# Performance work log

Hardware: AMD Instinct MI355X
Metric: run time of the kernel (lower is better)

Reference implementation:

```python
import jax, jax.numpy as jnp
import numpy as np

N = 4096        # batch size (rows)
K = 4           # instances per class -> num_instances in the torch code
D = 256         # embedding dim
MARGIN = 0.5
SAMPLE_KEY = jax.random.key(42)  # fixed key: deterministic stand-in for torch.multinomial


def setup_inputs() -> dict:
    key = jax.random.key(0)
    x = jax.random.normal(key, (N, D), dtype=jnp.float32)
    # L2-normalize like typical metric-learning embeddings so sims are in [-1, 1]
    inputs = x / jnp.linalg.norm(x, axis=1, keepdims=True)
    targets = (jnp.arange(N) // K).astype(jnp.int32)  # P*K batch: equal-size classes
    return {"inputs": inputs, "targets": targets}


def reference(inputs, targets):
    n = inputs.shape[0]
    km1 = K - 1                 # positives per row
    n_neg = n - K               # negatives per row

    sim = inputs @ inputs.T                                   # [n, n]
    same = targets[:, None] == targets[None, :]
    eye = jnp.eye(n, dtype=bool)
    pos_mask = same & ~eye
    neg_mask = ~same

    # masked_select + per-row sort: masked entries -> +inf, ascending sort,
    # keep first count entries (counts are uniform across rows)
    pos_sorted = jnp.sort(jnp.where(pos_mask, sim, jnp.inf), axis=1)[:, :km1]   # [n, K-1]
    neg_sorted = jnp.sort(jnp.where(neg_mask, sim, jnp.inf), axis=1)[:, :n_neg] # [n, n-K]

    pos_d = jnp.mean(pos_sorted)
    neg_d = jnp.mean(neg_sorted)

    # GaussDistribution per row over negatives
    neg_mean = jnp.mean(neg_sorted, axis=1, keepdims=True)
    neg_std = jnp.sqrt(jnp.mean((neg_sorted - neg_mean) ** 2, axis=1, keepdims=True))
    # NOTE: the original uses exp(+(x-mu)^2 / (2 sigma^2)) (no minus sign) -- faithful
    logprob = (neg_sorted - neg_mean) ** 2 / (2.0 * neg_std ** 2)               # [n, n-K]

    # multinomial without replacement ~ Gumbel top-k on log-weights
    gumbel = -jnp.log(-jnp.log(
        jax.random.uniform(SAMPLE_KEY, logprob.shape, minval=1e-20, maxval=1.0)))
    _, neg_idx = jax.lax.top_k(logprob + gumbel, km1)                            # [n, K-1]
    neg_pair = jnp.take_along_axis(neg_sorted, neg_idx, axis=1)                  # [n, K-1]

    pos_loss = jnp.mean(jnp.log1p(jnp.exp(-2.0 * (pos_sorted - MARGIN))), axis=1)
    neg_loss = 0.04 * jnp.mean(jnp.log1p(jnp.exp(50.0 * (neg_pair - MARGIN))), axis=1)
    loss = jnp.sum(pos_loss + neg_loss) / n

    # prec: fraction of rows where hardest positive > hardest sampled negative + 0.05
    c = jnp.sum(pos_sorted[:, -1] > jnp.max(neg_pair, axis=1) + 0.05)
    prec = c.astype(jnp.float32) / n

    return loss, prec, pos_d, neg_d
```

## Files before the change

kernel.cpp:

```cpp
#include <hip/hip_runtime.h>
#include <hip/hip_bf16.h>
#include <cstdint>
#include <cfloat>
#include <math.h>

#define NN 4096
#define DD 256
#define NNEG 4092
#define MARGIN 0.5f
#define NB 3584
#define NW (NB / 2)

__device__ __forceinline__ uint32_t rotl32(uint32_t x, int r) {
  return (x << r) | (x >> (32 - r));
}

__device__ __forceinline__ void threefry2x32_42(uint32_t x0, uint32_t x1,
                                                uint32_t& o0, uint32_t& o1) {
  const uint32_t k0 = 0u, k1 = 42u;
  const uint32_t k2 = k0 ^ k1 ^ 0x1BD11BDAu;
  x0 += k0; x1 += k1;
#define TF_R(r) { x0 += x1; x1 = rotl32(x1, r); x1 ^= x0; }
  TF_R(13) TF_R(15) TF_R(26) TF_R(6)
  x0 += k1; x1 += k2 + 1u;
  TF_R(17) TF_R(29) TF_R(16) TF_R(24)
  x0 += k2; x1 += k0 + 2u;
  TF_R(13) TF_R(15) TF_R(26) TF_R(6)
  x0 += k0; x1 += k1 + 3u;
  TF_R(17) TF_R(29) TF_R(16) TF_R(24)
  x0 += k1; x1 += k2 + 4u;
  TF_R(13) TF_R(15) TF_R(26) TF_R(6)
  x0 += k2; x1 += k0 + 5u;
#undef TF_R
  o0 = x0; o1 = x1;
}

__device__ __forceinline__ float gumbel_at(uint32_t f) {
  uint32_t o0, o1;
  threefry2x32_42(0u, f, o0, o1);
  uint32_t bits = o0 ^ o1;
  uint32_t fb = (bits >> 9) | 0x3F800000u;
  float fl = __uint_as_float(fb) - 1.0f;
  float u = fmaxf(1e-20f, fl + 1e-20f);
  return -logf(-logf(u));
}

__device__ __forceinline__ int bucket_of(float v) {
  return (int)fminf(fmaxf((v + 0.5f) * (float)NB, 0.0f), (float)(NB - 1));
}

#define BT 128
#define NT (NN / BT)
#define BK 32
#define LDSS 36

__global__ __launch_bounds__(256) void gemm_sim(const float* __restrict__ X,
                                                float* __restrict__ S) {
  __shared__ float As[BT * LDSS];
  __shared__ float Bs[BT * LDSS];
  const int tid = threadIdx.x;
  const int tx = tid & 15, ty = tid >> 4;

  int b = blockIdx.x, bi = 0;
  while (b >= NT - bi) { b -= NT - bi; bi++; }
  const int bj = bi + b;
  const int rowBase = bi * BT, colBase = bj * BT;

  float acc[8][8] = {};
  for (int kb = 0; kb < DD; kb += BK) {
#pragma unroll
    for (int it = 0; it < 4; ++it) {
      int idx = tid + 256 * it;
      int r = idx >> 3, c4 = idx & 7;
      float4 av = *(const float4*)(X + (size_t)(rowBase + r) * DD + kb + c4 * 4);
      float4 bv = *(const float4*)(X + (size_t)(colBase + r) * DD + kb + c4 * 4);
      *(float4*)(As + r * LDSS + c4 * 4) = av;
      *(float4*)(Bs + r * LDSS + c4 * 4) = bv;
    }
    __syncthreads();
    for (int k = 0; k < BK; k += 4) {
      float4 a[8], bfr[8];
#pragma unroll
      for (int i = 0; i < 8; ++i) a[i] = *(const float4*)(As + (ty + 16 * i) * LDSS + k);
#pragma unroll
      for (int j = 0; j < 8; ++j) bfr[j] = *(const float4*)(Bs + (tx + 16 * j) * LDSS + k);
#pragma unroll
      for (int i = 0; i < 8; ++i)
#pragma unroll
        for (int j = 0; j < 8; ++j) {
          acc[i][j] += a[i].x * bfr[j].x;
          acc[i][j] += a[i].y * bfr[j].y;
          acc[i][j] += a[i].z * bfr[j].z;
          acc[i][j] += a[i].w * bfr[j].w;
        }
    }
    __syncthreads();
  }
#pragma unroll
  for (int i = 0; i < 8; ++i)
#pragma unroll
    for (int j = 0; j < 8; ++j)
      S[(size_t)(rowBase + ty + 16 * i) * NN + colBase + tx + 16 * j] = acc[i][j];
  if (bi != bj) {
#pragma unroll
    for (int i = 0; i < 8; ++i)
#pragma unroll
      for (int j = 0; j < 8; ++j)
        S[(size_t)(colBase + tx + 16 * j) * NN + rowBase + ty + 16 * i] = acc[i][j];
  }
}

#define INSERT3(sc, v)                                              \
  if ((sc) > s2) {                                                  \
    if ((sc) > s1) {                                                \
      s2 = s1; v2 = v1;                                             \
      if ((sc) > s0) { s1 = s0; v1 = v0; s0 = (sc); v0 = (v); }     \
      else           { s1 = (sc); v1 = (v); }                       \
    } else { s2 = (sc); v2 = (v); }                                 \
  }

__global__ __launch_bounds__(256) void row_kernel(const float* __restrict__ S,
                                                  float* __restrict__ acc) {
  __shared__ uint32_t histw[NW];
  __shared__ uint32_t offsw[NW];
  __shared__ float sval[NN];
  __shared__ float sh[48];
  __shared__ uint32_t wtot[4];

  const int row = blockIdx.x;
  const int tid = threadIdx.x;
  const int lane = tid & 63, wid = tid >> 6;

#pragma unroll
  for (int i = 0; i < 7; ++i) histw[tid + 256 * i] = 0u;

  const float4* src = (const float4*)(S + (size_t)row * NN);
  const int pslot = row >> 2;
  float vv[16];
#pragma unroll
  for (int it = 0; it < 4; ++it) {
    int slot = tid + 256 * it;
    float4 t4 = src[slot];
    if (slot == pslot) {
      sh[16] = t4.x; sh[17] = t4.y; sh[18] = t4.z; sh[19] = t4.w;
      t4.x = INFINITY; t4.y = INFINITY; t4.z = INFINITY; t4.w = INFINITY;
    }
    vv[4 * it + 0] = t4.x; vv[4 * it + 1] = t4.y;
    vv[4 * it + 2] = t4.z; vv[4 * it + 3] = t4.w;
  }

  float s = 0.0f;
#pragma unroll
  for (int e = 0; e < 16; ++e) if (vv[e] < 1e30f) s += vv[e];
#pragma unroll
  for (int off = 32; off > 0; off >>= 1) s += __shfl_down(s, off, 64);
  if (lane == 0) sh[5 + wid] = s;
  __syncthreads();

#pragma unroll
  for (int e = 0; e < 16; ++e) {
    int b = bucket_of(vv[e]);
    atomicAdd(&histw[b >> 1], 1u << ((b & 1) << 4));
  }
  if (tid == 0) {
    int self = row & 3;
    float p[3]; int m = 0;
#pragma unroll
    for (int c = 0; c < 4; ++c)
      if (c != self) p[m++] = sh[16 + c];
    float t;
    if (p[0] > p[1]) { t = p[0]; p[0] = p[1]; p[1] = t; }
    if (p[1] > p[2]) { t = p[1]; p[1] = p[2]; p[2] = t; }
    if (p[0] > p[1]) { t = p[0]; p[0] = p[1]; p[1] = t; }
    sh[0] = p[0]; sh[1] = p[1]; sh[2] = p[2];
    float tot = sh[5] + sh[6] + sh[7] + sh[8];
    sh[9] = tot;
    sh[3] = tot / (float)NNEG;
  }
  __syncthreads();

  uint32_t hw[7];
  uint32_t s14 = 0;
#pragma unroll
  for (int j = 0; j < 7; ++j) {
    hw[j] = histw[7 * tid + j];
    s14 += (hw[j] & 0xFFFFu) + (hw[j] >> 16);
  }
  uint32_t inc = s14;
#pragma unroll
  for (int off = 1; off < 64; off <<= 1) {
    uint32_t n = __shfl_up(inc, (unsigned)off, 64);
    if (lane >= off) inc += n;
  }
  if (lane == 63) wtot[wid] = inc;

  const float mu = sh[3];
  float q = 0.0f;
#pragma unroll
  for (int e = 0; e < 16; ++e)
    if (vv[e] < 1e30f) { float d = vv[e] - mu; q += d * d; }
#pragma unroll
  for (int off = 32; off > 0; off >>= 1) q += __shfl_down(q, off, 64);
  if (lane == 0) sh[10 + wid] = q;
  __syncthreads();

  uint32_t wbase = 0;
  for (int w = 0; w < wid; ++w) wbase += wtot[w];
  uint32_t run = wbase + inc - s14;
#pragma unroll
  for (int j = 0; j < 7; ++j) {
    uint32_t lo = run; run += hw[j] & 0xFFFFu;
    uint32_t hi = run; run += hw[j] >> 16;
    offsw[7 * tid + j] = lo | (hi << 16);
  }
  if (tid == 0) {
    float var = (sh[10] + sh[11] + sh[12] + sh[13]) / (float)NNEG;
    float sd = sqrtf(var);
    sh[4] = 1.0f / (2.0f * sd * sd);
  }
  __syncthreads();

#pragma unroll
  for (int e = 0; e < 16; ++e) {
    int b = bucket_of(vv[e]);
    uint32_t old = atomicAdd(&offsw[b >> 1], 1u << ((b & 1) << 4));
    uint32_t sl = (old >> ((b & 1) << 4)) & 0xFFFFu;
    sval[sl] = vv[e];
  }
  __syncthreads();

  const float inv2s2 = sh[4];
  const uint32_t fbase = (uint32_t)row * (uint32_t)NNEG;
  float s0 = -FLT_MAX, s1 = -FLT_MAX, s2 = -FLT_MAX;
  float v0 = 0.0f, v1 = 0.0f, v2 = 0.0f;
#pragma unroll 1
  for (int it = 0; it < 16; ++it) {
    int sl = tid + 256 * it;
    float v = sval[sl];
    if (v < 1e30f) {
      int b = bucket_of(v);
      uint32_t sh16 = (uint32_t)((b & 1) << 4);
      uint32_t end = (offsw[b >> 1] >> sh16) & 0xFFFFu;
      uint32_t cntb = (histw[b >> 1] >> sh16) & 0xFFFFu;
      uint32_t st = end - cntb;
      int cnt = (int)st;
      for (uint32_t u = st; u < end; ++u) {
        float w = sval[u];
        cnt += (w < v || (w == v && (int)u < sl)) ? 1 : 0;
      }
      float d = v - mu;
      float sc = d * d * inv2s2 + gumbel_at(fbase + (uint32_t)cnt);
      INSERT3(sc, v)
    }
  }

#pragma unroll
  for (int dlt = 1; dlt < 64; dlt <<= 1) {
    float t0 = __shfl_xor(s0, dlt, 64), u0 = __shfl_xor(v0, dlt, 64);
    float t1 = __shfl_xor(s1, dlt, 64), u1 = __shfl_xor(v1, dlt, 64);
    float t2 = __shfl_xor(s2, dlt, 64), u2 = __shfl_xor(v2, dlt, 64);
    INSERT3(t0, u0)
    INSERT3(t1, u1)
    INSERT3(t2, u2)
  }
  if (lane == 0) {
    int b0 = 24 + wid * 6;
    sh[b0 + 0] = s0; sh[b0 + 1] = v0;
    sh[b0 + 2] = s1; sh[b0 + 3] = v1;
    sh[b0 + 4] = s2; sh[b0 + 5] = v2;
  }
  __syncthreads();

  if (tid == 0) {
    float g0 = -FLT_MAX, g1 = -FLT_MAX, g2 = -FLT_MAX;
    float w0 = 0.0f, w1 = 0.0f, w2 = 0.0f;
    {
      float s0 = g0, s1 = g1, s2 = g2, v0 = w0, v1 = w1, v2 = w2;
#pragma unroll
      for (int i = 0; i < 12; ++i) {
        float sc = sh[24 + 2 * i], v = sh[24 + 2 * i + 1];
        INSERT3(sc, v)
      }
      g0 = s0; g1 = s1; g2 = s2; w0 = v0; w1 = v1; w2 = v2;
    }
    float negmax = fmaxf(w0, fmaxf(w1, w2));
    float neg_loss = 0.04f * (log1pf(expf(50.0f * (w0 - MARGIN))) +
                              log1pf(expf(50.0f * (w1 - MARGIN))) +
                              log1pf(expf(50.0f * (w2 - MARGIN)))) / 3.0f;
    float p0 = sh[0], p1 = sh[1], p2 = sh[2];
    float pos_loss = (log1pf(expf(-2.0f * (p0 - MARGIN))) +
                      log1pf(expf(-2.0f * (p1 - MARGIN))) +
                      log1pf(expf(-2.0f * (p2 - MARGIN)))) / 3.0f;
    atomicAdd(&acc[0], pos_loss + neg_loss);
    if (p2 > negmax + 0.05f) atomicAdd(&acc[1], 1.0f);
    atomicAdd(&acc[2], p0 + p1 + p2);
    atomicAdd(&acc[3], sh[9]);
  }
}

__global__ void finalize(const float* __restrict__ acc, float* out) {
  if (threadIdx.x == 0 && blockIdx.x == 0) {
    out[0] = acc[0] / 4096.0f;
    out[1] = acc[1] / 4096.0f;
    out[2] = acc[2] / (4096.0f * 3.0f);
    out[3] = acc[3] / (4096.0f * 4092.0f);
  }
}

extern "C" void kernel_launch(void* const* d_in, const int* in_sizes, int n_in,
                              void* d_out, int out_size, void* d_ws, size_t ws_size,
                              hipStream_t stream) {
  (void)in_sizes; (void)n_in; (void)out_size; (void)ws_size;
  const float* X = (const float*)d_in[0];
  float* S = (float*)d_ws;
  float* acc = (float*)((char*)d_ws + (size_t)NN * NN * 4);
  hipMemsetAsync(acc, 0, 4 * sizeof(float), stream);
  gemm_sim<<<NT * (NT + 1) / 2, 256, 0, stream>>>(X, S);
  row_kernel<<<NN, 256, 0, stream>>>(S, acc);
  finalize<<<1, 64, 0, stream>>>(acc, (float*)d_out);
}
```

Before: 372.1 us.

## Precompute Gumbel noise table alongside GEMM and gather it in row kernel

Adds extra blocks to the GEMM launch that fill a full N×(N-K) table of Gumbel noise while the similarity GEMM runs. The row kernel then gathers the noise by rank instead of running threefry plus two logs per element, and its loop is split into a rank-count phase and a scoring phase to batch the loads. This swaps per-row transcendental compute for about 67MB of extra global writes and reads. The path runs only if the workspace is large enough, otherwise it falls back to generating noise inline.

```diff
diff --git a/kernel.cpp b/kernel.cpp
--- a/kernel.cpp
+++ b/kernel.cpp
@@ -53,12 +53,24 @@
 #define NT (NN / BT)
 #define BK 32
 #define LDSS 36
-
-__global__ __launch_bounds__(256) void gemm_sim(const float* __restrict__ X,
-                                                float* __restrict__ S) {
+#define GEMM_BLOCKS (NT * (NT + 1) / 2)
+#define GUMBEL_BLOCKS 240
+#define GTOTAL ((uint32_t)NN * (uint32_t)NNEG)
+
+__global__ __launch_bounds__(256) void gemm_gumbel(const float* __restrict__ X,
+                                                   float* __restrict__ S,
+                                                   float* __restrict__ G) {
   __shared__ float As[BT * LDSS];
   __shared__ float Bs[BT * LDSS];
   const int tid = threadIdx.x;
+
+  if (blockIdx.x >= GEMM_BLOCKS) {
+    uint32_t i = (uint32_t)(blockIdx.x - GEMM_BLOCKS) * 256u + (uint32_t)tid;
+    const uint32_t stride = (uint32_t)GUMBEL_BLOCKS * 256u;
+    for (; i < GTOTAL; i += stride) G[i] = gumbel_at(i);
+    return;
+  }
+
   const int tx = tid & 15, ty = tid >> 4;
 
   int b = blockIdx.x, bi = 0;
@@ -119,7 +131,9 @@
     } else { s2 = (sc); v2 = (v); }                                 \
   }
 
+template <int USE_G>
 __global__ __launch_bounds__(256) void row_kernel(const float* __restrict__ S,
+                                                  const float* __restrict__ G,
                                                   float* __restrict__ acc) {
   __shared__ uint32_t histw[NW];
   __shared__ uint32_t offsw[NW];
@@ -231,25 +245,38 @@
 
   const float inv2s2 = sh[4];
   const uint32_t fbase = (uint32_t)row * (uint32_t)NNEG;
+  const float* __restrict__ Grow = G + fbase;
   float s0 = -FLT_MAX, s1 = -FLT_MAX, s2 = -FLT_MAX;
   float v0 = 0.0f, v1 = 0.0f, v2 = 0.0f;
-#pragma unroll 1
+  float vr[16]; uint32_t cr[16];
+#pragma unroll
   for (int it = 0; it < 16; ++it) {
     int sl = tid + 256 * it;
     float v = sval[sl];
+    uint32_t cnt = 0u;
     if (v < 1e30f) {
       int b = bucket_of(v);
       uint32_t sh16 = (uint32_t)((b & 1) << 4);
       uint32_t end = (offsw[b >> 1] >> sh16) & 0xFFFFu;
       uint32_t cntb = (histw[b >> 1] >> sh16) & 0xFFFFu;
       uint32_t st = end - cntb;
-      int cnt = (int)st;
+      int c = (int)st;
       for (uint32_t u = st; u < end; ++u) {
         float w = sval[u];
-        cnt += (w < v || (w == v && (int)u < sl)) ? 1 : 0;
+        c += (w < v || (w == v && (int)u < sl)) ? 1 : 0;
       }
+      cnt = (uint32_t)c;
+    }
+    vr[it] = v; cr[it] = cnt;
+  }
+
+#pragma unroll
+  for (int it = 0; it < 16; ++it) {
+    float v = vr[it];
+    if (v < 1e30f) {
+      float g = USE_G ? Grow[cr[it]] : gumbel_at(fbase + cr[it]);
       float d = v - mu;
-      float sc = d * d * inv2s2 + gumbel_at(fbase + (uint32_t)cnt);
+      float sc = d * d * inv2s2 + g;
       INSERT3(sc, v)
     }
   }
@@ -310,12 +337,21 @@
 extern "C" void kernel_launch(void* const* d_in, const int* in_sizes, int n_in,
                               void* d_out, int out_size, void* d_ws, size_t ws_size,
                               hipStream_t stream) {
-  (void)in_sizes; (void)n_in; (void)out_size; (void)ws_size;
+  (void)in_sizes; (void)n_in; (void)out_size;
   const float* X = (const float*)d_in[0];
   float* S = (float*)d_ws;
   float* acc = (float*)((char*)d_ws + (size_t)NN * NN * 4);
+  float* G = (float*)((char*)d_ws + (size_t)NN * NN * 4 + 256);
+  const size_t need = (size_t)NN * NN * 4 + 256 + (size_t)GTOTAL * 4;
+  const bool have_g = ws_size >= need;
+
   hipMemsetAsync(acc, 0, 4 * sizeof(float), stream);
-  gemm_sim<<<NT * (NT + 1) / 2, 256, 0, stream>>>(X, S);
-  row_kernel<<<NN, 256, 0, stream>>>(S, acc);
+  if (have_g) {
+    gemm_gumbel<<<GEMM_BLOCKS + GUMBEL_BLOCKS, 256, 0, stream>>>(X, S, G);
+    row_kernel<1><<<NN, 256, 0, stream>>>(S, G, acc);
+  } else {
+    gemm_gumbel<<<GEMM_BLOCKS, 256, 0, stream>>>(X, S, G);
+    row_kernel<0><<<NN, 256, 0, stream>>>(S, G, acc);
+  }
   finalize<<<1, 64, 0, stream>>>(acc, (float*)d_out);
 }
```

Result: no change. 374.8 us (+0.7%).
